# Performance work log

Measured on AMD Instinct MI355X. Metric: run time of the kernel, lower is better.

## Reference

```python
import jax, jax.numpy as jnp
import numpy as np

EPS = 1e-5

def _conv3x3(x, w, b):
    y = jax.lax.conv_general_dilated(x, w, window_strides=(1, 1),
                                     padding=((1, 1), (1, 1)),
                                     dimension_numbers=('NCHW', 'OIHW', 'NCHW'))
    return y + b[None, :, None, None]

def _bilinear_gather(x, py, px):
    # x: [B,C,H,W]; py,px: [B,K,H,W] absolute sampling coords; zero outside image (DCN convention).
    B, C, H, W = x.shape
    Kk = py.shape[1]
    y0 = jnp.floor(py)
    x0 = jnp.floor(px)
    ly = py - y0
    lx = px - x0
    y0i = y0.astype(jnp.int32)
    x0i = x0.astype(jnp.int32)
    xf = x.reshape(B, C, H * W)

    def gather(yi, xi):
        valid = (yi >= 0) & (yi < H) & (xi >= 0) & (xi < W)
        idx = (jnp.clip(yi, 0, H - 1) * W + jnp.clip(xi, 0, W - 1)).reshape(B, -1)
        g = jax.vmap(lambda xb, ib: xb[:, ib])(xf, idx).reshape(B, C, Kk, H, W)
        return g * valid[:, None].astype(x.dtype)

    v00 = gather(y0i, x0i)
    v01 = gather(y0i, x0i + 1)
    v10 = gather(y0i + 1, x0i)
    v11 = gather(y0i + 1, x0i + 1)
    ly = ly[:, None]
    lx = lx[:, None]
    return (v00 * (1 - ly) * (1 - lx) + v01 * (1 - ly) * lx
            + v10 * ly * (1 - lx) + v11 * ly * lx)

def _shift_forward(x, w_off, b_off, w_conv, b_conv, gamma, beta, run_mean, run_var):
    B, C, H, W = x.shape
    om = _conv3x3(x, w_off, b_off)              # [B,27,H,W] offset/mask predictor
    dy = om[:, 0:18:2]                          # [B,9,H,W] per-tap y offsets
    dx = om[:, 1:18:2]                          # [B,9,H,W] per-tap x offsets
    mask = jax.nn.sigmoid(om[:, 18:27])         # [B,9,H,W] modulation (DCNv2)
    kk = jnp.arange(3, dtype=x.dtype) - 1.0     # kernel tap offsets for 3x3, dilation 1
    ky = jnp.repeat(kk, 3)                      # [9]
    kx = jnp.tile(kk, 3)                        # [9]
    hh = jnp.arange(H, dtype=x.dtype)
    ww = jnp.arange(W, dtype=x.dtype)
    py = hh[None, None, :, None] + ky[None, :, None, None] + dy
    px = ww[None, None, None, :] + kx[None, :, None, None] + dx
    s = _bilinear_gather(x, py, px) * mask[:, None]   # [B,C,9,H,W]
    Co = w_conv.shape[0]
    y = jnp.einsum('bckhw,ock->bohw', s, w_conv.reshape(Co, C, 9))
    y = y + b_conv[None, :, None, None]
    # BatchNorm2d (inference) + ReLU, then residual add
    inv = jax.lax.rsqrt(run_var + EPS)
    y = (y - run_mean[None, :, None, None]) * (inv * gamma)[None, :, None, None] + beta[None, :, None, None]
    y = jax.nn.relu(y)
    return x + y

def setup_inputs():
    key = jax.random.key(0)
    ks = jax.random.split(key, 3)
    B, C, H, W = 2, 256, 96, 96
    x = jax.random.normal(ks[0], (B, C, H, W), dtype=jnp.float32)
    w_off = jax.random.normal(ks[1], (27, C, 3, 3), dtype=jnp.float32) * 0.01
    b_off = jnp.zeros((27,), dtype=jnp.float32)
    w_conv = jax.random.normal(ks[2], (C, C, 3, 3), dtype=jnp.float32) * 0.02
    b_conv = jnp.zeros((C,), dtype=jnp.float32)
    gamma = jnp.ones((C,), dtype=jnp.float32)
    beta = jnp.zeros((C,), dtype=jnp.float32)
    run_mean = jnp.zeros((C,), dtype=jnp.float32)
    run_var = jnp.ones((C,), dtype=jnp.float32)
    return {"x": x, "w_off": w_off, "b_off": b_off, "w_conv": w_conv,
            "b_conv": b_conv, "gamma": gamma, "beta": beta,
            "run_mean": run_mean, "run_var": run_var}

def reference(x, w_off, b_off, w_conv, b_conv, gamma, beta, run_mean, run_var):
    return _shift_forward(x, w_off, b_off, w_conv, b_conv, gamma, beta, run_mean, run_var)
```

## Files before the change

### kernel.cpp

```cpp
#include <hip/hip_runtime.h>
#include <hip/hip_bf16.h>

#define H_ 96
#define W_ 96
#define HW_ 9216
#define C_ 256
#define KO_ 27
#define EPS_ 1e-5f

typedef unsigned short u16;
typedef unsigned short ushort8 __attribute__((ext_vector_type(8)));
typedef unsigned short ushort4v __attribute__((ext_vector_type(4)));
typedef short short8v __attribute__((ext_vector_type(8)));
typedef float float4v __attribute__((ext_vector_type(4)));

__device__ __forceinline__ float b2f(u16 u) {
    return __uint_as_float(((unsigned int)u) << 16);
}
__device__ __forceinline__ u16 f2b(float f) {
    __hip_bfloat16 h = __float2bfloat16(f);
    union { __hip_bfloat16 h; u16 u; } cv; cv.h = h; return cv.u;
}
__device__ __forceinline__ unsigned int pack2(float a, float b) {
    union { __hip_bfloat162 h; unsigned int u; } cv;
    cv.h = __float22bfloat162_rn(make_float2(a, b));
    return cv.u;
}
__device__ __forceinline__ void glds16(const u16* g, u16* l) {
    __builtin_amdgcn_global_load_lds(
        (const __attribute__((address_space(1))) void*)g,
        (__attribute__((address_space(3))) void*)l, 16, 0, 0);
}

__global__ __launch_bounds__(256) void prep_kernel(
    const float* __restrict__ x,
    const float* __restrict__ w_conv, const float* __restrict__ w_off,
    const float* __restrict__ b_conv,
    const float* __restrict__ gamma, const float* __restrict__ beta,
    const float* __restrict__ rmean, const float* __restrict__ rvar,
    float* __restrict__ AB, u16* __restrict__ WQ, u16* __restrict__ WO,
    u16* __restrict__ XT)
{
    __shared__ u16 sbuf[3200];
    const int bx = blockIdx.x;
    const int tid = threadIdx.x;

    if (bx < 384) {
        u16 (*ls)[100] = (u16 (*)[100])sbuf;
        int h    = bx % 96;
        int t2   = bx / 96;
        int b    = t2 >> 1;
        int half = t2 & 1;
        for (int cgi = 0; cgi < 4; ++cgi) {
            int c0 = (half * 4 + cgi) * 32;
            for (int e = tid; e < 32 * W_; e += 256) {
                int ci = e / W_, w = e % W_;
                ls[ci][w] = f2b(x[((b * C_ + c0 + ci) * H_ + h) * W_ + w]);
            }
            __syncthreads();
            for (int u = tid; u < 768; u += 256) {
                int g4 = u & 7, w = u >> 3;
                ushort4v v;
#pragma unroll
                for (int t = 0; t < 4; t++) v[t] = ls[g4 * 4 + t][w];
                *(ushort4v*)&XT[((b * H_ + h) * W_ + w) * C_ + c0 + g4 * 4] = v;
            }
            __syncthreads();
        }
    } else if (bx < 640) {
        int o = bx - 384;
        for (int i = tid; i < 2304; i += 256)
            sbuf[i] = f2b(w_conv[o * 2304 + i]);
        __syncthreads();
        int cg = tid >> 5, ln = tid & 31;
#pragma unroll
        for (int k = 0; k < 9; ++k)
            WQ[(k * 8 + cg) * 8192 + o * 32 + ln] = sbuf[(cg * 32 + ln) * 9 + k];
    } else if (bx < 672) {
        int o = bx - 640;
        for (int i = tid; i < 2304; i += 256)
            sbuf[i] = (o < KO_) ? f2b(w_off[o * 2304 + i]) : (u16)0;
        __syncthreads();
        int cg = tid >> 5, ln = tid & 31;
#pragma unroll
        for (int k = 0; k < 9; ++k)
            WO[(k * 8 + cg) * 1024 + o * 32 + ln] = sbuf[(cg * 32 + ln) * 9 + k];
    } else {
        int o = tid;
        float sc = gamma[o] * rsqrtf(rvar[o] + EPS_);
        AB[o] = sc;
        AB[256 + o] = beta[o] + (b_conv[o] - rmean[o]) * sc;
    }
}

__global__ __launch_bounds__(256) void offsets_kernel(
    const u16* __restrict__ XT, const u16* __restrict__ WO,
    const float* __restrict__ b_off, float* __restrict__ OFF)
{
    __shared__ float red[4][2][32][17];

    const int tid  = threadIdx.x;
    const int wave = tid >> 6;
    const int lane = tid & 63;
    const int quad = lane >> 4;
    const int l15  = lane & 15;

    const int n0 = blockIdx.x * 32;
    const int b  = n0 / HW_;
    const int p0 = n0 - b * HW_;
    const int h  = p0 / W_;
    const int w0 = p0 % W_;

    float4v oa[2][2];
#pragma unroll
    for (int ph = 0; ph < 2; ph++)
#pragma unroll
        for (int hh = 0; hh < 2; hh++)
            oa[ph][hh] = float4v{0.f, 0.f, 0.f, 0.f};

    int basec0 = 0, basec1 = 0; bool vld0 = true, vld1 = true;
    auto oset = [&](int tap) {
        int py = h + tap / 3 - 1;
        bool vy = (unsigned)py < (unsigned)H_;
        int pyc = min(max(py, 0), H_ - 1);
        int rowb = (b * H_ + pyc) * W_;
        {
            int pxl = w0 + l15 + tap % 3 - 1;
            vld0 = vy && ((unsigned)pxl < (unsigned)W_);
            basec0 = (rowb + min(max(pxl, 0), W_ - 1)) * C_ + quad * 8;
        }
        {
            int pxl = w0 + 16 + l15 + tap % 3 - 1;
            vld1 = vy && ((unsigned)pxl < (unsigned)W_);
            basec1 = (rowb + min(max(pxl, 0), W_ - 1)) * C_ + quad * 8;
        }
    };
    auto bld0 = [&](int c32) -> ushort8 {
        ushort8 v = *(const ushort8*)(XT + basec0 + (c32 & 7) * 32);
#pragma unroll
        for (int j = 0; j < 8; j++) v[j] = vld0 ? v[j] : (u16)0;
        return v;
    };
    auto bld1 = [&](int c32) -> ushort8 {
        ushort8 v = *(const ushort8*)(XT + basec1 + (c32 & 7) * 32);
#pragma unroll
        for (int j = 0; j < 8; j++) v[j] = vld1 ? v[j] : (u16)0;
        return v;
    };
    const int i0 = wave * 18, i1 = i0 + 18;
    int curtap = i0 >> 3;
    oset(curtap);
    ushort8 b0 = bld0(i0), b1 = bld1(i0);
    short8v wa = *(const short8v*)(WO + i0 * 1024 + l15 * 32 + quad * 8);
    short8v wb = *(const short8v*)(WO + i0 * 1024 + l15 * 32 + quad * 8 + 512);
    for (int i = i0; i < i1; ++i) {
        ushort8 c0v = b0, c1v = b1;
        short8v wac = wa, wbc = wb;
        int nx = i + 1;
        if (nx < i1) {
            int t = nx >> 3;
            if (t != curtap) { oset(t); curtap = t; }
            b0 = bld0(nx); b1 = bld1(nx);
            wa = *(const short8v*)(WO + nx * 1024 + l15 * 32 + quad * 8);
            wb = *(const short8v*)(WO + nx * 1024 + l15 * 32 + quad * 8 + 512);
        }
        union { ushort8 u; short8v s; } u0, u1; u0.u = c0v; u1.u = c1v;
        oa[0][0] = __builtin_amdgcn_mfma_f32_16x16x32_bf16(wac, u0.s, oa[0][0], 0, 0, 0);
        oa[0][1] = __builtin_amdgcn_mfma_f32_16x16x32_bf16(wbc, u0.s, oa[0][1], 0, 0, 0);
        oa[1][0] = __builtin_amdgcn_mfma_f32_16x16x32_bf16(wac, u1.s, oa[1][0], 0, 0, 0);
        oa[1][1] = __builtin_amdgcn_mfma_f32_16x16x32_bf16(wbc, u1.s, oa[1][1], 0, 0, 0);
    }
#pragma unroll
    for (int r = 0; r < 4; ++r) {
        red[wave][0][quad * 4 + r][l15]      = oa[0][0][r];
        red[wave][0][16 + quad * 4 + r][l15] = oa[0][1][r];
        red[wave][1][quad * 4 + r][l15]      = oa[1][0][r];
        red[wave][1][16 + quad * 4 + r][l15] = oa[1][1][r];
    }
    __syncthreads();
    for (int u = tid; u < 1024; u += 256) {
        int px = u & 31, o = u >> 5;
        if (o < KO_) {
            int ph = px >> 4, pp = px & 15;
            float v = red[0][ph][o][pp] + red[1][ph][o][pp]
                    + red[2][ph][o][pp] + red[3][ph][o][pp] + b_off[o];
            OFF[(size_t)(n0 + px) * 32 + o] =
                (o < 18) ? v : 1.f / (1.f + expf(-v));
        }
    }
}

__global__ __launch_bounds__(256) void fused_kernel(
    const float* __restrict__ x, const u16* __restrict__ XT,
    const float* __restrict__ OFF, const u16* __restrict__ WQ,
    const float* __restrict__ AB, float* __restrict__ out)
{
    __shared__ __align__(16) u16 sA[8192];
    __shared__ __align__(16) u16 sB[2048];
    __shared__ float offv[32][32];

    const int tid  = threadIdx.x;
    const int wave = tid >> 6;
    const int lane = tid & 63;
    const int quad = lane >> 4;
    const int l15  = lane & 15;

    const int bid = blockIdx.x;
    const int swz = (bid & 7) * 144 + (bid >> 3);
    const int o0  = (swz & 1) << 7;
    const int n0  = (swz >> 1) * 32;
    const int b   = n0 / HW_;
    const int p0  = n0 - b * HW_;
    const int h   = p0 / W_;
    const int w0  = p0 % W_;

    {
        int px = tid >> 3, q4 = (tid & 7) * 4;
        float4 v = *(const float4*)(OFF + (size_t)(n0 + px) * 32 + q4);
        *(float4*)&offv[px][q4] = v;
    }
    __syncthreads();

    float4v acc[2][2];
#pragma unroll
    for (int i = 0; i < 2; i++)
#pragma unroll
        for (int jj = 0; jj < 2; jj++)
            acc[i][jj] = float4v{0.f, 0.f, 0.f, 0.f};

    const int le8 = lane * 8;
    const int wo  = wave * 32;

    const int ppx = tid >> 3;
    const int pj  = tid & 7;
    const int sboff = (pj >> 2) * 1024 + ppx * 32 + (pj & 3) * 8;

    float fc0, fc1, fc2, fc3, fn0, fn1, fn2, fn3;
    int a00, a01, a10, a11;

    auto tap_setup = [&](int tap) {
        float dy = offv[ppx][2 * tap];
        float dx = offv[ppx][2 * tap + 1];
        float m  = offv[ppx][18 + tap];
        float py  = (float)(h + tap / 3 - 1) + dy;
        float pxx = (float)(w0 + ppx + tap % 3 - 1) + dx;
        float y0f = floorf(py), x0f = floorf(pxx);
        float ly = py - y0f, lx = pxx - x0f;
        int y0 = (int)y0f, x0i = (int)x0f;
        int y1 = y0 + 1, x1 = x0i + 1;
        bool vy0 = (unsigned)y0 < (unsigned)H_;
        bool vy1 = (unsigned)y1 < (unsigned)H_;
        bool vx0 = (unsigned)x0i < (unsigned)W_;
        bool vx1 = (unsigned)x1 < (unsigned)W_;
        fn0 = (vy0 && vx0) ? (1.f - ly) * (1.f - lx) * m : 0.f;
        fn1 = (vy0 && vx1) ? (1.f - ly) * lx * m : 0.f;
        fn2 = (vy1 && vx0) ? ly * (1.f - lx) * m : 0.f;
        fn3 = (vy1 && vx1) ? ly * lx * m : 0.f;
        int y0c = min(max(y0, 0), H_ - 1), y1c = min(max(y1, 0), H_ - 1);
        int x0c = min(max(x0i, 0), W_ - 1), x1c = min(max(x1, 0), W_ - 1);
        a00 = ((b * H_ + y0c) * W_ + x0c) * C_;
        a01 = ((b * H_ + y0c) * W_ + x1c) * C_;
        a10 = ((b * H_ + y1c) * W_ + x0c) * C_;
        a11 = ((b * H_ + y1c) * W_ + x1c) * C_;
    };
    auto stageA = [&](int tap, int q) {
#pragma unroll
        for (int i = 0; i < 4; ++i) {
            int unit = i * 4 + wave;
            int cc = unit >> 3;
            glds16(WQ + (size_t)(tap * 8 + q * 2 + cc) * 8192 + o0 * 32
                      + (unit & 7) * 512 + le8,
                   &sA[unit * 512]);
        }
    };

    tap_setup(0);
    fc0 = fn0; fc1 = fn1; fc2 = fn2; fc3 = fn3;
    ushort8 gc00 = *(const ushort8*)(XT + a00 + pj * 8);
    ushort8 gc01 = *(const ushort8*)(XT + a01 + pj * 8);
    ushort8 gc10 = *(const ushort8*)(XT + a10 + pj * 8);
    ushort8 gc11 = *(const ushort8*)(XT + a11 + pj * 8);
    stageA(0, 0);
    ushort8 gn00{}, gn01{}, gn10{}, gn11{};

#pragma unroll 4
    for (int ch = 0; ch < 36; ++ch) {
        {
            float v[8];
#pragma unroll
            for (int t = 0; t < 8; t++)
                v[t] = fc0 * b2f(gc00[t]) + fc1 * b2f(gc01[t])
                     + fc2 * b2f(gc10[t]) + fc3 * b2f(gc11[t]);
            uint4 sv;
            sv.x = pack2(v[0], v[1]);
            sv.y = pack2(v[2], v[3]);
            sv.z = pack2(v[4], v[5]);
            sv.w = pack2(v[6], v[7]);
            *(uint4*)&sB[sboff] = sv;
        }
        asm volatile("s_waitcnt vmcnt(0) lgkmcnt(0)" ::: "memory");
        __builtin_amdgcn_s_barrier();

        short8v af[2][2], bfr[2][2];
#pragma unroll
        for (int cc = 0; cc < 2; ++cc) {
#pragma unroll
            for (int mt = 0; mt < 2; ++mt)
                af[cc][mt] = *(const short8v*)
                    &sA[cc * 4096 + (wo + mt * 16 + l15) * 32 + quad * 8];
#pragma unroll
            for (int nt = 0; nt < 2; ++nt)
                bfr[cc][nt] = *(const short8v*)
                    &sB[cc * 1024 + (nt * 16 + l15) * 32 + quad * 8];
        }
        asm volatile("s_waitcnt lgkmcnt(0)" ::: "memory");
        __builtin_amdgcn_s_barrier();

        if (ch < 35) {
            const int chn = ch + 1, tapn = chn >> 2, qn = chn & 3;
            if (qn == 0) tap_setup(tapn);
            const int cb = qn * 64 + pj * 8;
            gn00 = *(const ushort8*)(XT + a00 + cb);
            gn01 = *(const ushort8*)(XT + a01 + cb);
            gn10 = *(const ushort8*)(XT + a10 + cb);
            gn11 = *(const ushort8*)(XT + a11 + cb);
            stageA(tapn, qn);
        }
        __builtin_amdgcn_s_setprio(1);
#pragma unroll
        for (int cc = 0; cc < 2; ++cc)
#pragma unroll
            for (int mt = 0; mt < 2; ++mt)
#pragma unroll
                for (int nt = 0; nt < 2; ++nt)
                    acc[mt][nt] = __builtin_amdgcn_mfma_f32_16x16x32_bf16(
                        af[cc][mt], bfr[cc][nt], acc[mt][nt], 0, 0, 0);
        __builtin_amdgcn_s_setprio(0);
        gc00 = gn00; gc01 = gn01; gc10 = gn10; gc11 = gn11;
        fc0 = fn0; fc1 = fn1; fc2 = fn2; fc3 = fn3;
    }

    const float* Ao = AB;
    const float* Bo = AB + 256;
#pragma unroll
    for (int mt = 0; mt < 2; mt++) {
#pragma unroll
        for (int nt = 0; nt < 2; nt++) {
            int pix = p0 + nt * 16 + l15;
#pragma unroll
            for (int r = 0; r < 4; r++) {
                int o = o0 + wo + mt * 16 + quad * 4 + r;
                float v = acc[mt][nt][r] * Ao[o] + Bo[o];
                v = fmaxf(v, 0.f);
                int gi = (b * C_ + o) * HW_ + pix;
                out[gi] = x[gi] + v;
            }
        }
    }
}

extern "C" void kernel_launch(void* const* d_in, const int* in_sizes, int n_in,
                              void* d_out, int out_size, void* d_ws, size_t ws_size,
                              hipStream_t stream)
{
    (void)in_sizes; (void)n_in; (void)out_size; (void)ws_size;
    const float* x      = (const float*)d_in[0];
    const float* w_off  = (const float*)d_in[1];
    const float* b_off  = (const float*)d_in[2];
    const float* w_conv = (const float*)d_in[3];
    const float* b_conv = (const float*)d_in[4];
    const float* gamma  = (const float*)d_in[5];
    const float* beta   = (const float*)d_in[6];
    const float* rmean  = (const float*)d_in[7];
    const float* rvar   = (const float*)d_in[8];
    float* out = (float*)d_out;

    float* ws = (float*)d_ws;
    float* AB = ws;
    u16* WQ = (u16*)(AB + 512);
    u16* WO = WQ + 589824;
    u16* XT = WO + 73728;
    float* OFF = (float*)(XT + 4718592);

    prep_kernel<<<673, 256, 0, stream>>>(x, w_conv, w_off, b_conv, gamma, beta,
                                         rmean, rvar, AB, WQ, WO, XT);
    offsets_kernel<<<576, 256, 0, stream>>>(XT, WO, b_off, OFF);
    fused_kernel<<<1152, 256, 0, stream>>>(x, XT, OFF, WQ, AB, out);
}
```

Before: 195.3 us.

## Enlarge fused kernel tile to all 256 output channels by 64 pixels

Each block of the fused deformable-conv GEMM kernel now covers all 256 output channels and 64 pixels with 512 threads, instead of 128 channels by 32 pixels with 256 threads. The bilinear sampling of each pixel is now done once rather than repeated for both output-channel halves, which removes redundant gather and interpolation work and raises MFMA work per staged tile. The cost is fewer blocks (288), more LDS and accumulator registers per block, and possibly lower occupancy and weaker latency hiding.

```diff
diff --git a/kernel.cpp b/kernel.cpp
--- a/kernel.cpp
+++ b/kernel.cpp
@@ -190,14 +190,14 @@
     }
 }
 
-__global__ __launch_bounds__(256) void fused_kernel(
+__global__ __launch_bounds__(512) void fused_kernel(
     const float* __restrict__ x, const u16* __restrict__ XT,
     const float* __restrict__ OFF, const u16* __restrict__ WQ,
     const float* __restrict__ AB, float* __restrict__ out)
 {
-    __shared__ __align__(16) u16 sA[8192];
-    __shared__ __align__(16) u16 sB[2048];
-    __shared__ float offv[32][32];
+    __shared__ __align__(16) u16 sA[16384];
+    __shared__ __align__(16) u16 sB[4096];
+    __shared__ float offv[64][36];
 
     const int tid  = threadIdx.x;
     const int wave = tid >> 6;
@@ -206,44 +206,46 @@
     const int l15  = lane & 15;
 
     const int bid = blockIdx.x;
-    const int swz = (bid & 7) * 144 + (bid >> 3);
-    const int o0  = (swz & 1) << 7;
-    const int n0  = (swz >> 1) * 32;
+    const int swz = (bid & 7) * 36 + (bid >> 3);
+    const int n0  = swz * 64;
     const int b   = n0 / HW_;
     const int p0  = n0 - b * HW_;
-    const int h   = p0 / W_;
-    const int w0  = p0 % W_;
+
+    const int wo = (wave & 3) * 64;
+    const int wp = (wave >> 2) * 32;
+
+    const int pj    = tid & 7;
+    const int ptile = ((tid >> 3) & 31) | ((tid >> 8) << 5);
+    const int pixt  = p0 + ptile;
+    const int hp    = pixt / W_;
+    const int wpx   = pixt % W_;
+    const int sboff = (pj >> 2) * 2048 + ptile * 32 + (pj & 3) * 8;
 
     {
-        int px = tid >> 3, q4 = (tid & 7) * 4;
-        float4 v = *(const float4*)(OFF + (size_t)(n0 + px) * 32 + q4);
-        *(float4*)&offv[px][q4] = v;
+        int i = tid >> 3, j4 = (tid & 7) * 4;
+        float4 v = *(const float4*)(OFF + (size_t)(n0 + i) * 32 + j4);
+        *(float4*)&offv[i][j4] = v;
     }
     __syncthreads();
 
-    float4v acc[2][2];
-#pragma unroll
-    for (int i = 0; i < 2; i++)
+    float4v acc[4][2];
+#pragma unroll
+    for (int i = 0; i < 4; i++)
 #pragma unroll
         for (int jj = 0; jj < 2; jj++)
             acc[i][jj] = float4v{0.f, 0.f, 0.f, 0.f};
 
     const int le8 = lane * 8;
-    const int wo  = wave * 32;
-
-    const int ppx = tid >> 3;
-    const int pj  = tid & 7;
-    const int sboff = (pj >> 2) * 1024 + ppx * 32 + (pj & 3) * 8;
 
     float fc0, fc1, fc2, fc3, fn0, fn1, fn2, fn3;
     int a00, a01, a10, a11;
 
     auto tap_setup = [&](int tap) {
-        float dy = offv[ppx][2 * tap];
-        float dx = offv[ppx][2 * tap + 1];
-        float m  = offv[ppx][18 + tap];
-        float py  = (float)(h + tap / 3 - 1) + dy;
-        float pxx = (float)(w0 + ppx + tap % 3 - 1) + dx;
+        float dy = offv[ptile][2 * tap];
+        float dx = offv[ptile][2 * tap + 1];
+        float m  = offv[ptile][18 + tap];
+        float py  = (float)(hp + tap / 3 - 1) + dy;
+        float pxx = (float)(wpx + tap % 3 - 1) + dx;
         float y0f = floorf(py), x0f = floorf(pxx);
         float ly = py - y0f, lx = pxx - x0f;
         int y0 = (int)y0f, x0i = (int)x0f;
@@ -266,10 +268,10 @@
     auto stageA = [&](int tap, int q) {
 #pragma unroll
         for (int i = 0; i < 4; ++i) {
-            int unit = i * 4 + wave;
-            int cc = unit >> 3;
-            glds16(WQ + (size_t)(tap * 8 + q * 2 + cc) * 8192 + o0 * 32
-                      + (unit & 7) * 512 + le8,
+            int unit = i * 8 + wave;
+            int cc = unit >> 4;
+            glds16(WQ + (size_t)(tap * 8 + q * 2 + cc) * 8192
+                      + (unit & 15) * 512 + le8,
                    &sA[unit * 512]);
         }
     };
@@ -301,17 +303,17 @@
         asm volatile("s_waitcnt vmcnt(0) lgkmcnt(0)" ::: "memory");
         __builtin_amdgcn_s_barrier();
 
-        short8v af[2][2], bfr[2][2];
+        short8v af[2][4], bfr[2][2];
 #pragma unroll
         for (int cc = 0; cc < 2; ++cc) {
 #pragma unroll
-            for (int mt = 0; mt < 2; ++mt)
+            for (int mt = 0; mt < 4; ++mt)
                 af[cc][mt] = *(const short8v*)
-                    &sA[cc * 4096 + (wo + mt * 16 + l15) * 32 + quad * 8];
+                    &sA[cc * 8192 + (wo + mt * 16 + l15) * 32 + quad * 8];
 #pragma unroll
             for (int nt = 0; nt < 2; ++nt)
                 bfr[cc][nt] = *(const short8v*)
-                    &sB[cc * 1024 + (nt * 16 + l15) * 32 + quad * 8];
+                    &sB[cc * 2048 + (wp + nt * 16 + l15) * 32 + quad * 8];
         }
         asm volatile("s_waitcnt lgkmcnt(0)" ::: "memory");
         __builtin_amdgcn_s_barrier();
@@ -330,7 +332,7 @@
 #pragma unroll
         for (int cc = 0; cc < 2; ++cc)
 #pragma unroll
-            for (int mt = 0; mt < 2; ++mt)
+            for (int mt = 0; mt < 4; ++mt)
 #pragma unroll
                 for (int nt = 0; nt < 2; ++nt)
                     acc[mt][nt] = __builtin_amdgcn_mfma_f32_16x16x32_bf16(
@@ -343,13 +345,13 @@
     const float* Ao = AB;
     const float* Bo = AB + 256;
 #pragma unroll
-    for (int mt = 0; mt < 2; mt++) {
+    for (int mt = 0; mt < 4; mt++) {
 #pragma unroll
         for (int nt = 0; nt < 2; nt++) {
-            int pix = p0 + nt * 16 + l15;
+            int pix = p0 + wp + nt * 16 + l15;
 #pragma unroll
             for (int r = 0; r < 4; r++) {
-                int o = o0 + wo + mt * 16 + quad * 4 + r;
+                int o = wo + mt * 16 + quad * 4 + r;
                 float v = acc[mt][nt][r] * Ao[o] + Bo[o];
                 v = fmaxf(v, 0.f);
                 int gi = (b * C_ + o) * HW_ + pix;
@@ -385,5 +387,5 @@
     prep_kernel<<<673, 256, 0, stream>>>(x, w_conv, w_off, b_conv, gamma, beta,
                                          rmean, rvar, AB, WQ, WO, XT);
     offsets_kernel<<<576, 256, 0, stream>>>(XT, WO, b_off, OFF);
-    fused_kernel<<<1152, 256, 0, stream>>>(x, XT, OFF, WQ, AB, out);
-}
+    fused_kernel<<<288, 512, 0, stream>>>(x, XT, OFF, WQ, AB, out);
+}
```

Measured after the change: 226.1 us. 15.8% more time.

## Fuse offset predictor into deformable conv kernel and widen output tile to all channels

Applied to the files above, without the earlier changes.

Merges the offset/mask conv into the main fused kernel, so each block computes its 32 pixels' offsets into shared memory instead of writing and re-reading an OFF buffer through a separate launch. Each block now covers all 256 output channels (4x2 MFMA tiles per wave) rather than half, so the offsets and the bilinear gather are computed once per pixel tile instead of twice. The NCHW to NHWC transpose in prep is also restructured to read float4 rows per channel and write 16-byte vectors. The trade-off is higher register use, more LDS per block, and half as many blocks, which can lower occupancy.

```diff
diff --git a/kernel.cpp b/kernel.cpp
--- a/kernel.cpp
+++ b/kernel.cpp
@@ -41,50 +41,55 @@
     float* __restrict__ AB, u16* __restrict__ WQ, u16* __restrict__ WO,
     u16* __restrict__ XT)
 {
-    __shared__ u16 sbuf[3200];
+    __shared__ __align__(16) u16 sbuf[32][264];
     const int bx = blockIdx.x;
     const int tid = threadIdx.x;
 
-    if (bx < 384) {
-        u16 (*ls)[100] = (u16 (*)[100])sbuf;
-        int h    = bx % 96;
-        int t2   = bx / 96;
-        int b    = t2 >> 1;
-        int half = t2 & 1;
-        for (int cgi = 0; cgi < 4; ++cgi) {
-            int c0 = (half * 4 + cgi) * 32;
-            for (int e = tid; e < 32 * W_; e += 256) {
-                int ci = e / W_, w = e % W_;
-                ls[ci][w] = f2b(x[((b * C_ + c0 + ci) * H_ + h) * W_ + w]);
-            }
-            __syncthreads();
-            for (int u = tid; u < 768; u += 256) {
-                int g4 = u & 7, w = u >> 3;
-                ushort4v v;
-#pragma unroll
-                for (int t = 0; t < 4; t++) v[t] = ls[g4 * 4 + t][w];
-                *(ushort4v*)&XT[((b * H_ + h) * W_ + w) * C_ + c0 + g4 * 4] = v;
-            }
-            __syncthreads();
-        }
-    } else if (bx < 640) {
-        int o = bx - 384;
+    if (bx < 576) {
+        const int seg = bx % 3, hh = (bx / 3) % 96, bb = bx / 288;
+        const int w0s = seg * 32;
+        {
+            const int c = tid;
+            const float* xp = x + ((bb * C_ + c) * H_ + hh) * W_ + w0s;
+            float4 xv[8];
+#pragma unroll
+            for (int j = 0; j < 8; j++) xv[j] = *(const float4*)(xp + j * 4);
+#pragma unroll
+            for (int j = 0; j < 8; j++) {
+                sbuf[j * 4 + 0][c] = f2b(xv[j].x);
+                sbuf[j * 4 + 1][c] = f2b(xv[j].y);
+                sbuf[j * 4 + 2][c] = f2b(xv[j].z);
+                sbuf[j * 4 + 3][c] = f2b(xv[j].w);
+            }
+        }
+        __syncthreads();
+#pragma unroll
+        for (int it = 0; it < 4; ++it) {
+            int u = it * 256 + tid;
+            int px = u >> 5, slot = u & 31;
+            ushort8 v = *(const ushort8*)&sbuf[px][slot * 8];
+            *(ushort8*)&XT[((bb * H_ + hh) * W_ + w0s + px) * C_ + slot * 8] = v;
+        }
+    } else if (bx < 832) {
+        int o = bx - 576;
+        u16* flat = &sbuf[0][0];
         for (int i = tid; i < 2304; i += 256)
-            sbuf[i] = f2b(w_conv[o * 2304 + i]);
+            flat[i] = f2b(w_conv[o * 2304 + i]);
         __syncthreads();
         int cg = tid >> 5, ln = tid & 31;
 #pragma unroll
         for (int k = 0; k < 9; ++k)
-            WQ[(k * 8 + cg) * 8192 + o * 32 + ln] = sbuf[(cg * 32 + ln) * 9 + k];
-    } else if (bx < 672) {
-        int o = bx - 640;
+            WQ[(k * 8 + cg) * 8192 + o * 32 + ln] = flat[(cg * 32 + ln) * 9 + k];
+    } else if (bx < 864) {
+        int o = bx - 832;
+        u16* flat = &sbuf[0][0];
         for (int i = tid; i < 2304; i += 256)
-            sbuf[i] = (o < KO_) ? f2b(w_off[o * 2304 + i]) : (u16)0;
+            flat[i] = (o < KO_) ? f2b(w_off[o * 2304 + i]) : (u16)0;
         __syncthreads();
         int cg = tid >> 5, ln = tid & 31;
 #pragma unroll
         for (int k = 0; k < 9; ++k)
-            WO[(k * 8 + cg) * 1024 + o * 32 + ln] = sbuf[(cg * 32 + ln) * 9 + k];
+            WO[(k * 8 + cg) * 1024 + o * 32 + ln] = flat[(cg * 32 + ln) * 9 + k];
     } else {
         int o = tid;
         float sc = gamma[o] * rsqrtf(rvar[o] + EPS_);
@@ -93,11 +98,17 @@
     }
 }
 
-__global__ __launch_bounds__(256) void offsets_kernel(
-    const u16* __restrict__ XT, const u16* __restrict__ WO,
-    const float* __restrict__ b_off, float* __restrict__ OFF)
+__global__ __launch_bounds__(256) void fused_kernel(
+    const float* __restrict__ x, const u16* __restrict__ XT,
+    const u16* __restrict__ WO, const float* __restrict__ b_off,
+    const u16* __restrict__ WQ, const float* __restrict__ AB,
+    float* __restrict__ out)
 {
-    __shared__ float red[4][2][32][17];
+    __shared__ __align__(16) unsigned char smem[41472];
+    u16*   sA   = (u16*)smem;
+    u16*   sB   = (u16*)(smem + 32768);
+    float* offv = (float*)(smem + 36864);
+    float (*red)[2][32][17] = (float (*)[2][32][17])smem;
 
     const int tid  = threadIdx.x;
     const int wave = tid >> 6;
@@ -105,77 +116,81 @@
     const int quad = lane >> 4;
     const int l15  = lane & 15;
 
-    const int n0 = blockIdx.x * 32;
-    const int b  = n0 / HW_;
-    const int p0 = n0 - b * HW_;
-    const int h  = p0 / W_;
-    const int w0 = p0 % W_;
-
-    float4v oa[2][2];
-#pragma unroll
-    for (int ph = 0; ph < 2; ph++)
-#pragma unroll
-        for (int hh = 0; hh < 2; hh++)
-            oa[ph][hh] = float4v{0.f, 0.f, 0.f, 0.f};
-
-    int basec0 = 0, basec1 = 0; bool vld0 = true, vld1 = true;
-    auto oset = [&](int tap) {
-        int py = h + tap / 3 - 1;
-        bool vy = (unsigned)py < (unsigned)H_;
-        int pyc = min(max(py, 0), H_ - 1);
-        int rowb = (b * H_ + pyc) * W_;
-        {
-            int pxl = w0 + l15 + tap % 3 - 1;
-            vld0 = vy && ((unsigned)pxl < (unsigned)W_);
-            basec0 = (rowb + min(max(pxl, 0), W_ - 1)) * C_ + quad * 8;
-        }
-        {
-            int pxl = w0 + 16 + l15 + tap % 3 - 1;
-            vld1 = vy && ((unsigned)pxl < (unsigned)W_);
-            basec1 = (rowb + min(max(pxl, 0), W_ - 1)) * C_ + quad * 8;
-        }
-    };
-    auto bld0 = [&](int c32) -> ushort8 {
-        ushort8 v = *(const ushort8*)(XT + basec0 + (c32 & 7) * 32);
-#pragma unroll
-        for (int j = 0; j < 8; j++) v[j] = vld0 ? v[j] : (u16)0;
-        return v;
-    };
-    auto bld1 = [&](int c32) -> ushort8 {
-        ushort8 v = *(const ushort8*)(XT + basec1 + (c32 & 7) * 32);
-#pragma unroll
-        for (int j = 0; j < 8; j++) v[j] = vld1 ? v[j] : (u16)0;
-        return v;
-    };
-    const int i0 = wave * 18, i1 = i0 + 18;
-    int curtap = i0 >> 3;
-    oset(curtap);
-    ushort8 b0 = bld0(i0), b1 = bld1(i0);
-    short8v wa = *(const short8v*)(WO + i0 * 1024 + l15 * 32 + quad * 8);
-    short8v wb = *(const short8v*)(WO + i0 * 1024 + l15 * 32 + quad * 8 + 512);
-    for (int i = i0; i < i1; ++i) {
-        ushort8 c0v = b0, c1v = b1;
-        short8v wac = wa, wbc = wb;
-        int nx = i + 1;
-        if (nx < i1) {
-            int t = nx >> 3;
-            if (t != curtap) { oset(t); curtap = t; }
-            b0 = bld0(nx); b1 = bld1(nx);
-            wa = *(const short8v*)(WO + nx * 1024 + l15 * 32 + quad * 8);
-            wb = *(const short8v*)(WO + nx * 1024 + l15 * 32 + quad * 8 + 512);
-        }
-        union { ushort8 u; short8v s; } u0, u1; u0.u = c0v; u1.u = c1v;
-        oa[0][0] = __builtin_amdgcn_mfma_f32_16x16x32_bf16(wac, u0.s, oa[0][0], 0, 0, 0);
-        oa[0][1] = __builtin_amdgcn_mfma_f32_16x16x32_bf16(wbc, u0.s, oa[0][1], 0, 0, 0);
-        oa[1][0] = __builtin_amdgcn_mfma_f32_16x16x32_bf16(wac, u1.s, oa[1][0], 0, 0, 0);
-        oa[1][1] = __builtin_amdgcn_mfma_f32_16x16x32_bf16(wbc, u1.s, oa[1][1], 0, 0, 0);
-    }
-#pragma unroll
-    for (int r = 0; r < 4; ++r) {
-        red[wave][0][quad * 4 + r][l15]      = oa[0][0][r];
-        red[wave][0][16 + quad * 4 + r][l15] = oa[0][1][r];
-        red[wave][1][quad * 4 + r][l15]      = oa[1][0][r];
-        red[wave][1][16 + quad * 4 + r][l15] = oa[1][1][r];
+    const int bid = blockIdx.x;
+    const int swz = (bid & 7) * 72 + (bid >> 3);
+    const int n0  = swz * 32;
+    const int b   = n0 / HW_;
+    const int p0  = n0 - b * HW_;
+    const int h   = p0 / W_;
+    const int w0  = p0 % W_;
+
+    {
+        float4v oa[2][2];
+#pragma unroll
+        for (int ph = 0; ph < 2; ph++)
+#pragma unroll
+            for (int hh = 0; hh < 2; hh++)
+                oa[ph][hh] = float4v{0.f, 0.f, 0.f, 0.f};
+
+        int basec0 = 0, basec1 = 0; bool vld0 = true, vld1 = true;
+        auto oset = [&](int tap) {
+            int py = h + tap / 3 - 1;
+            bool vy = (unsigned)py < (unsigned)H_;
+            int pyc = min(max(py, 0), H_ - 1);
+            int rowb = (b * H_ + pyc) * W_;
+            {
+                int pxl = w0 + l15 + tap % 3 - 1;
+                vld0 = vy && ((unsigned)pxl < (unsigned)W_);
+                basec0 = (rowb + min(max(pxl, 0), W_ - 1)) * C_ + quad * 8;
+            }
+            {
+                int pxl = w0 + 16 + l15 + tap % 3 - 1;
+                vld1 = vy && ((unsigned)pxl < (unsigned)W_);
+                basec1 = (rowb + min(max(pxl, 0), W_ - 1)) * C_ + quad * 8;
+            }
+        };
+        auto bld0 = [&](int c32) -> ushort8 {
+            ushort8 v = *(const ushort8*)(XT + basec0 + (c32 & 7) * 32);
+#pragma unroll
+            for (int j = 0; j < 8; j++) v[j] = vld0 ? v[j] : (u16)0;
+            return v;
+        };
+        auto bld1 = [&](int c32) -> ushort8 {
+            ushort8 v = *(const ushort8*)(XT + basec1 + (c32 & 7) * 32);
+#pragma unroll
+            for (int j = 0; j < 8; j++) v[j] = vld1 ? v[j] : (u16)0;
+            return v;
+        };
+        const int i0 = wave * 18, i1 = i0 + 18;
+        int curtap = i0 >> 3;
+        oset(curtap);
+        ushort8 b0 = bld0(i0), b1 = bld1(i0);
+        short8v wa = *(const short8v*)(WO + i0 * 1024 + l15 * 32 + quad * 8);
+        short8v wb = *(const short8v*)(WO + i0 * 1024 + l15 * 32 + quad * 8 + 512);
+        for (int i = i0; i < i1; ++i) {
+            ushort8 c0v = b0, c1v = b1;
+            short8v wac = wa, wbc = wb;
+            int nx = i + 1;
+            if (nx < i1) {
+                int t = nx >> 3;
+                if (t != curtap) { oset(t); curtap = t; }
+                b0 = bld0(nx); b1 = bld1(nx);
+                wa = *(const short8v*)(WO + nx * 1024 + l15 * 32 + quad * 8);
+                wb = *(const short8v*)(WO + nx * 1024 + l15 * 32 + quad * 8 + 512);
+            }
+            union { ushort8 u; short8v s; } u0, u1; u0.u = c0v; u1.u = c1v;
+            oa[0][0] = __builtin_amdgcn_mfma_f32_16x16x32_bf16(wac, u0.s, oa[0][0], 0, 0, 0);
+            oa[0][1] = __builtin_amdgcn_mfma_f32_16x16x32_bf16(wbc, u0.s, oa[0][1], 0, 0, 0);
+            oa[1][0] = __builtin_amdgcn_mfma_f32_16x16x32_bf16(wac, u1.s, oa[1][0], 0, 0, 0);
+            oa[1][1] = __builtin_amdgcn_mfma_f32_16x16x32_bf16(wbc, u1.s, oa[1][1], 0, 0, 0);
+        }
+#pragma unroll
+        for (int r = 0; r < 4; ++r) {
+            red[wave][0][quad * 4 + r][l15]      = oa[0][0][r];
+            red[wave][0][16 + quad * 4 + r][l15] = oa[0][1][r];
+            red[wave][1][quad * 4 + r][l15]      = oa[1][0][r];
+            red[wave][1][16 + quad * 4 + r][l15] = oa[1][1][r];
+        }
     }
     __syncthreads();
     for (int u = tid; u < 1024; u += 256) {
@@ -184,52 +199,20 @@
             int ph = px >> 4, pp = px & 15;
             float v = red[0][ph][o][pp] + red[1][ph][o][pp]
                     + red[2][ph][o][pp] + red[3][ph][o][pp] + b_off[o];
-            OFF[(size_t)(n0 + px) * 32 + o] =
-                (o < 18) ? v : 1.f / (1.f + expf(-v));
-        }
-    }
-}
-
-__global__ __launch_bounds__(256) void fused_kernel(
-    const float* __restrict__ x, const u16* __restrict__ XT,
-    const float* __restrict__ OFF, const u16* __restrict__ WQ,
-    const float* __restrict__ AB, float* __restrict__ out)
-{
-    __shared__ __align__(16) u16 sA[8192];
-    __shared__ __align__(16) u16 sB[2048];
-    __shared__ float offv[32][32];
-
-    const int tid  = threadIdx.x;
-    const int wave = tid >> 6;
-    const int lane = tid & 63;
-    const int quad = lane >> 4;
-    const int l15  = lane & 15;
-
-    const int bid = blockIdx.x;
-    const int swz = (bid & 7) * 144 + (bid >> 3);
-    const int o0  = (swz & 1) << 7;
-    const int n0  = (swz >> 1) * 32;
-    const int b   = n0 / HW_;
-    const int p0  = n0 - b * HW_;
-    const int h   = p0 / W_;
-    const int w0  = p0 % W_;
-
-    {
-        int px = tid >> 3, q4 = (tid & 7) * 4;
-        float4 v = *(const float4*)(OFF + (size_t)(n0 + px) * 32 + q4);
-        *(float4*)&offv[px][q4] = v;
+            offv[px * 36 + o] = (o < 18) ? v : 1.f / (1.f + expf(-v));
+        }
     }
     __syncthreads();
 
-    float4v acc[2][2];
-#pragma unroll
-    for (int i = 0; i < 2; i++)
+    float4v acc[4][2];
+#pragma unroll
+    for (int i = 0; i < 4; i++)
 #pragma unroll
         for (int jj = 0; jj < 2; jj++)
             acc[i][jj] = float4v{0.f, 0.f, 0.f, 0.f};
 
     const int le8 = lane * 8;
-    const int wo  = wave * 32;
+    const int wo  = wave * 64;
 
     const int ppx = tid >> 3;
     const int pj  = tid & 7;
@@ -239,9 +222,9 @@
     int a00, a01, a10, a11;
 
     auto tap_setup = [&](int tap) {
-        float dy = offv[ppx][2 * tap];
-        float dx = offv[ppx][2 * tap + 1];
-        float m  = offv[ppx][18 + tap];
+        float dy = offv[ppx * 36 + 2 * tap];
+        float dx = offv[ppx * 36 + 2 * tap + 1];
+        float m  = offv[ppx * 36 + 18 + tap];
         float py  = (float)(h + tap / 3 - 1) + dy;
         float pxx = (float)(w0 + ppx + tap % 3 - 1) + dx;
         float y0f = floorf(py), x0f = floorf(pxx);
@@ -265,11 +248,11 @@
     };
     auto stageA = [&](int tap, int q) {
 #pragma unroll
-        for (int i = 0; i < 4; ++i) {
+        for (int i = 0; i < 8; ++i) {
             int unit = i * 4 + wave;
-            int cc = unit >> 3;
-            glds16(WQ + (size_t)(tap * 8 + q * 2 + cc) * 8192 + o0 * 32
-                      + (unit & 7) * 512 + le8,
+            int cc = unit >> 4;
+            glds16(WQ + (size_t)(tap * 8 + q * 2 + cc) * 8192
+                      + (unit & 15) * 512 + le8,
                    &sA[unit * 512]);
         }
     };
@@ -301,13 +284,13 @@
         asm volatile("s_waitcnt vmcnt(0) lgkmcnt(0)" ::: "memory");
         __builtin_amdgcn_s_barrier();
 
-        short8v af[2][2], bfr[2][2];
+        short8v af[2][4], bfr[2][2];
 #pragma unroll
         for (int cc = 0; cc < 2; ++cc) {
 #pragma unroll
-            for (int mt = 0; mt < 2; ++mt)
+            for (int mt = 0; mt < 4; ++mt)
                 af[cc][mt] = *(const short8v*)
-                    &sA[cc * 4096 + (wo + mt * 16 + l15) * 32 + quad * 8];
+                    &sA[cc * 8192 + (wo + mt * 16 + l15) * 32 + quad * 8];
 #pragma unroll
             for (int nt = 0; nt < 2; ++nt)
                 bfr[cc][nt] = *(const short8v*)
@@ -330,7 +313,7 @@
 #pragma unroll
         for (int cc = 0; cc < 2; ++cc)
 #pragma unroll
-            for (int mt = 0; mt < 2; ++mt)
+            for (int mt = 0; mt < 4; ++mt)
 #pragma unroll
                 for (int nt = 0; nt < 2; ++nt)
                     acc[mt][nt] = __builtin_amdgcn_mfma_f32_16x16x32_bf16(
@@ -343,13 +326,13 @@
     const float* Ao = AB;
     const float* Bo = AB + 256;
 #pragma unroll
-    for (int mt = 0; mt < 2; mt++) {
+    for (int mt = 0; mt < 4; mt++) {
 #pragma unroll
         for (int nt = 0; nt < 2; nt++) {
             int pix = p0 + nt * 16 + l15;
 #pragma unroll
             for (int r = 0; r < 4; r++) {
-                int o = o0 + wo + mt * 16 + quad * 4 + r;
+                int o = wo + mt * 16 + quad * 4 + r;
                 float v = acc[mt][nt][r] * Ao[o] + Bo[o];
                 v = fmaxf(v, 0.f);
                 int gi = (b * C_ + o) * HW_ + pix;
@@ -380,10 +363,8 @@
     u16* WQ = (u16*)(AB + 512);
     u16* WO = WQ + 589824;
     u16* XT = WO + 73728;
-    float* OFF = (float*)(XT + 4718592);
-
-    prep_kernel<<<673, 256, 0, stream>>>(x, w_conv, w_off, b_conv, gamma, beta,
+
+    prep_kernel<<<865, 256, 0, stream>>>(x, w_conv, w_off, b_conv, gamma, beta,
                                          rmean, rvar, AB, WQ, WO, XT);
-    offsets_kernel<<<576, 256, 0, stream>>>(XT, WO, b_off, OFF);
-    fused_kernel<<<1152, 256, 0, stream>>>(x, XT, OFF, WQ, AB, out);
-}
+    fused_kernel<<<576, 256, 0, stream>>>(x, XT, WO, b_off, WQ, AB, out);
+}
```

Result: faster. 171.9 us (-12.0%).
